# Kernel optimization log

Hardware: AMD Instinct MI355X
Metric: run time of the kernel (lower is better)

## Reference

```python
import jax, jax.numpy as jnp
import numpy as np

NEURON_CDECAY = 0.5
NEURON_VDECAY = 0.75
NEURON_VTH = 0.5
PSEUDO_WINDOW = 0.5

@jax.custom_vjp
def pseudo_spike(v):
    return (v > NEURON_VTH).astype(v.dtype)

def _ps_fwd(v):
    return pseudo_spike(v), v

def _ps_bwd(v, g):
    return (g * (jnp.abs(v - NEURON_VTH) < PSEUDO_WINDOW).astype(g.dtype),)

pseudo_spike.defvjp(_ps_fwd, _ps_bwd)

def clif_scan(X_tbd):
    # X_tbd: [T, B, D] synaptic inputs; CLIF neuron recurrence over time.
    def step(carry, x_t):
        c, v, s = carry
        c = c * NEURON_CDECAY + x_t
        v = v * NEURON_VDECAY * (1.0 - s) + c
        s = pseudo_spike(v)
        return (c, v, s), s
    z = jnp.zeros(X_tbd.shape[1:], X_tbd.dtype)
    _, spikes = jax.lax.scan(step, (z, z, z), X_tbd)
    return spikes  # [T, B, D]

def setup_inputs() -> dict:
    key = jax.random.key(0)
    ks = jax.random.split(key, 8)
    B, IN, H1, H2, OUT, T = 256, 2048, 2048, 2048, 1024, 16
    def lin(k, fan_in, fan_out):
        bound = 1.0 / np.sqrt(fan_in)
        kw, kb = jax.random.split(k)
        W = jax.random.uniform(kw, (fan_out, fan_in), jnp.float32, -bound, bound)
        b = jax.random.uniform(kb, (fan_out,), jnp.float32, -bound, bound)
        return W, b
    W0, b0 = lin(ks[0], IN, H1)
    W1, b1 = lin(ks[1], H1, H2)
    W_out, b_out = lin(ks[2], H2, OUT)
    in_pop_spikes = (jax.random.uniform(ks[3], (B, IN, T), jnp.float32) < 0.5).astype(jnp.float32)
    return {"in_pop_spikes": in_pop_spikes, "W0": W0, "b0": b0, "W1": W1, "b1": b1,
            "W_out": W_out, "b_out": b_out, "batch_size": B, "update": 0, "re_calibration": 0}

def reference(in_pop_spikes, W0, b0, W1, b1, W_out, b_out, batch_size, update, re_calibration):
    # layer 0: linear over all timesteps, then CLIF scan
    x = jnp.moveaxis(in_pop_spikes, -1, 0)                    # [T, B, IN]
    s0 = clif_scan(jnp.einsum('tbi,hi->tbh', x, W0) + b0)     # [T, B, H1]
    s1 = clif_scan(jnp.einsum('tbh,gh->tbg', s0, W1) + b1)    # [T, B, H2]
    so = clif_scan(jnp.einsum('tbg,og->tbo', s1, W_out) + b_out)  # [T, B, OUT]
    return jnp.mean(so, axis=0)  # out_pop_act: sum over T / spike_ts
```

## Files before the change

### kernel.cpp

```cpp
#include <hip/hip_runtime.h>
#include <stdint.h>


typedef int v4i __attribute__((ext_vector_type(4)));
typedef int v16i __attribute__((ext_vector_type(16)));

#define TT 16
constexpr int KD = 2048;
constexpr double SCALE = 268435456.0;
constexpr double BAND = 3.5e-5;
constexpr uint32_t FCAP = 262144;

#define GLOAD_LDS16(g, s)                                                      \
  __builtin_amdgcn_global_load_lds(                                            \
      (const __attribute__((address_space(1))) uint32_t*)(g),                  \
      (__attribute__((address_space(3))) uint32_t*)(s), 16, 0, 0)

__device__ __forceinline__ size_t af_addr(int m, int k) {
  return ((size_t)((m >> 5) * 64 + (k >> 5)) << 10)
       + ((size_t)((m & 31) + (((k >> 4) & 1) << 5)) << 4) + (k & 15);
}

__global__ __launch_bounds__(256)
void prep_all(const float* __restrict__ W0, const float* __restrict__ W1,
              const float* __restrict__ Wo, int8_t* __restrict__ F0,
              int8_t* __restrict__ F1, int8_t* __restrict__ Fo,
              const float* __restrict__ X, int8_t* __restrict__ AF0,
              uint32_t* fl0, uint32_t* fl1, uint32_t* fl2) {
  if (blockIdx.x == 0 && threadIdx.x < 3) {
    if (threadIdx.x == 0) fl0[0] = 0;
    else if (threadIdx.x == 1) fl1[0] = 0;
    else fl2[0] = 0;
  }
  int blk = blockIdx.x;
  if (blk >= 2560) {
    const int idx = (blk - 2560) * 256 + threadIdx.x;
    const float4* src = reinterpret_cast<const float4*>(X) + (size_t)idx * 4;
    float4 v[4];
    v[0] = src[0]; v[1] = src[1]; v[2] = src[2]; v[3] = src[3];
    const float* f = reinterpret_cast<const float*>(v);
    const int b = idx >> 11, i = idx & 2047;
    const size_t base = af_addr(b * TT, i);
#pragma unroll
    for (int t = 0; t < TT; ++t) AF0[base + (size_t)t * 16] = (int8_t)f[t];
    return;
  }
  const float* W;
  int8_t* dst;
  int total;
  if (blk < 1024)      { W = W0; dst = F0; total = 2048 * 2048; }
  else if (blk < 2048) { W = W1; dst = F1; total = 2048 * 2048; blk -= 1024; }
  else                 { W = Wo; dst = Fo; total = 1024 * 2048; blk -= 2048; }
  const int g = blk * 256 + threadIdx.x;
  const int lane = g & 63;
  const int n = ((g >> 12) << 5) + (lane & 31);
  const int k0 = (((g & 4095) >> 6) << 5) + ((lane >> 5) << 4);
  const float* src = W + (size_t)n * 2048 + k0;
  float4 wv[4];
#pragma unroll
  for (int q = 0; q < 4; ++q) wv[q] = *reinterpret_cast<const float4*>(src + q * 4);
  const float* f = reinterpret_cast<const float*>(wv);
  long long nn[16];
#pragma unroll
  for (int e = 0; e < 16; ++e) nn[e] = (long long)rint((double)f[e] * SCALE);
  const size_t base = (size_t)g * 16;
#pragma unroll
  for (int l = 0; l < 3; ++l) {
    alignas(16) char c[16];
#pragma unroll
    for (int e = 0; e < 16; ++e) {
      const int d = (int)((nn[e] + 128) & 255) - 128;
      c[e] = (char)d;
      nn[e] = (nn[e] - d) >> 8;
    }
    *reinterpret_cast<v4i*>(dst + (size_t)l * total + base) = *(const v4i*)c;
  }
}

static __device__ __forceinline__ v16i zero16() {
  v16i z;
#pragma unroll
  for (int i = 0; i < 16; ++i) z[i] = 0;
  return z;
}

template<int N, bool FINAL>
__global__ __launch_bounds__(256, 2)
void gemm_scan_i8(const int8_t* __restrict__ AF,
                  const int8_t* __restrict__ WF,
                  const float* __restrict__ bias,
                  void* __restrict__ outp,
                  uint32_t* __restrict__ fb) {
  __shared__ union SM {
    int8_t buf[3][20 * 1024];
    double c[4][32 * 33];
  } sm;

  const int tid = threadIdx.x;
  const int lane = tid & 63;
  const int w = tid >> 6;
  const int wy = w >> 1, nsub = w & 1;

  if ((blockIdx.x >> 8) & 1) asm volatile("s_sleep 16");

  constexpr int NN = N / 64;
  constexpr int NWG = 32 * NN;
  const int h = blockIdx.x;
  const int wk = (h & 7) * (NWG >> 3) + (h >> 3);
  const int panel = wk >> 6;
  const int within = wk & 63;
  const int mt = (panel & 3) * 8 + (within & 7);
  const int nt = (panel >> 2) * 8 + (within >> 3);
  const int m0 = mt * 128;
  const int n0 = nt * 64;
  const size_t lst = (size_t)N * KD;

  const int8_t* asrc[2];
  int adst[2];
#pragma unroll
  for (int j = 0; j < 2; ++j) {
    const int fa = w + 4 * j;
    asrc[j] = AF + ((size_t)(((m0 >> 5) + (fa >> 1)) * 64 + (fa & 1)) << 10)
            + lane * 16;
    adst[j] = fa * 1024;
  }
  const int8_t* bsrc[3];
  int bdst[3];
#pragma unroll
  for (int j = 0; j < 3; ++j) {
    const int f = w + 4 * j;
    const int l = f >> 2, kk = (f >> 1) & 1, ns = f & 1;
    bsrc[j] = WF + (size_t)l * lst
            + ((size_t)(((n0 >> 5) + ns) * 64 + kk) << 10) + lane * 16;
    bdst[j] = (8 + f) * 1024;
  }

  v16i acc[3][2];
#pragma unroll
  for (int l = 0; l < 3; ++l) { acc[l][0] = zero16(); acc[l][1] = zero16(); }

  constexpr int NT2 = KD / 64;

#pragma unroll
  for (int j = 0; j < 2; ++j) GLOAD_LDS16(asrc[j], &sm.buf[0][adst[j]]);
#pragma unroll
  for (int j = 0; j < 3; ++j) GLOAD_LDS16(bsrc[j], &sm.buf[0][bdst[j]]);
#pragma unroll
  for (int j = 0; j < 2; ++j) GLOAD_LDS16(asrc[j] + 2048, &sm.buf[1][adst[j]]);
#pragma unroll
  for (int j = 0; j < 3; ++j) GLOAD_LDS16(bsrc[j] + 2048, &sm.buf[1][bdst[j]]);

#define GATE()                                                                 \
  __builtin_amdgcn_s_barrier();                                                \
  asm volatile("s_waitcnt lgkmcnt(0)" ::: "memory");                           \
  __builtin_amdgcn_sched_barrier(0)

#define MFMA4(L, BF)                                                           \
  __builtin_amdgcn_s_setprio(1);                                               \
  acc[L][0] = __builtin_amdgcn_mfma_i32_32x32x32_i8(afr[0][0], BF[0], acc[L][0], 0, 0, 0); \
  acc[L][1] = __builtin_amdgcn_mfma_i32_32x32x32_i8(afr[1][0], BF[0], acc[L][1], 0, 0, 0); \
  acc[L][0] = __builtin_amdgcn_mfma_i32_32x32x32_i8(afr[0][1], BF[1], acc[L][0], 0, 0, 0); \
  acc[L][1] = __builtin_amdgcn_mfma_i32_32x32x32_i8(afr[1][1], BF[1], acc[L][1], 0, 0, 0); \
  __builtin_amdgcn_s_setprio(0)

#define BREAD(BF, L)                                                           \
  BF[0] = *(const v4i*)(bb + ((8 + (((L) << 2) | nsub)) << 10) + lane * 16);   \
  BF[1] = *(const v4i*)(bb + ((8 + (((L) << 2) | 2 | nsub)) << 10) + lane * 16)

  int bufc = 0;
  for (int t2 = 0; t2 < NT2; ++t2) {
    if (t2 == NT2 - 1) asm volatile("s_waitcnt vmcnt(0)" ::: "memory");
    else               asm volatile("s_waitcnt vmcnt(5)" ::: "memory");
    __builtin_amdgcn_s_barrier();
    const int8_t* bb = sm.buf[bufc];
    int b2 = bufc + 2; if (b2 >= 3) b2 -= 3;
    const bool stage = (t2 + 2 < NT2);
    const size_t soff = (size_t)(t2 + 2) * 2048;

    v4i afr[2][2], bf0[2], bf1[2];
    if (stage) {
      GLOAD_LDS16(asrc[0] + soff, &sm.buf[b2][adst[0]]);
      GLOAD_LDS16(asrc[1] + soff, &sm.buf[b2][adst[1]]);
    }
#pragma unroll
    for (int mi = 0; mi < 2; ++mi)
#pragma unroll
      for (int kk = 0; kk < 2; ++kk)
        afr[mi][kk] = *(const v4i*)(bb + ((((wy * 2 + mi) << 1) | kk) << 10)
                                       + lane * 16);
    BREAD(bf0, 0);
    GATE();
    MFMA4(0, bf0);

    if (stage) {
      GLOAD_LDS16(bsrc[0] + soff, &sm.buf[b2][bdst[0]]);
      GLOAD_LDS16(bsrc[1] + soff, &sm.buf[b2][bdst[1]]);
    }
    BREAD(bf1, 1);
    GATE();
    MFMA4(1, bf1);

    if (stage) {
      GLOAD_LDS16(bsrc[2] + soff, &sm.buf[b2][bdst[2]]);
    }
    BREAD(bf0, 2);
    GATE();
    MFMA4(2, bf0);

    ++bufc; if (bufc == 3) bufc = 0;
  }
#undef BREAD
#undef MFMA4
#undef GATE

  const int rep = (lane & 31) * 0x01010101;
  v4i rowv; rowv[0] = rep; rowv[1] = rep; rowv[2] = rep; rowv[3] = rep;
  v4i onev; onev[0] = 0x01010101; onev[1] = 0x01010101;
            onev[2] = 0x01010101; onev[3] = 0x01010101;
  const v16i drow = __builtin_amdgcn_mfma_i32_32x32x32_i8(rowv, onev, zero16(), 0, 0, 0);
  const v16i dcol = __builtin_amdgcn_mfma_i32_32x32x32_i8(onev, rowv, zero16(), 0, 0, 0);

  const int col = lane & 31;
  const int bl = lane >> 5;
  double* cw = sm.c[w];
#pragma unroll
  for (int mi = 0; mi < 2; ++mi) {
    __syncthreads();
#pragma unroll
    for (int i = 0; i < 16; ++i) {
      long long ts = acc[2][mi][i];
      ts = (ts << 8) + acc[1][mi][i];
      ts = (ts << 8) + acc[0][mi][i];
      cw[(drow[i] >> 5) * 33 + (dcol[i] >> 5)] = (double)ts * 0x1p-28;
    }
    __syncthreads();

    const int gn = n0 + nsub * 32 + col;
    const int gm = m0 + (wy * 2 + mi) * 32 + bl * 16;
    const double bj = (double)bias[gn];
    double cc = 0.0, vv = 0.0, ss = 0.0;
    int flg = 0;
    if (!FINAL) {
      int8_t* so = (int8_t*)outp;
      const size_t ab = af_addr(gm, gn);
#pragma unroll
      for (int t = 0; t < TT; ++t) {
        const double x = cw[(bl * 16 + t) * 33 + col] + bj;
        cc = cc * 0.5 + x;
        vv = vv * 0.75 * (1.0 - ss) + cc;
        ss = (vv > 0.5) ? 1.0 : 0.0;
        flg |= (fabs(vv - 0.5) < BAND);
        so[ab + (size_t)t * 16] = (int8_t)ss;
      }
    } else {
      float tot = 0.0f;
#pragma unroll
      for (int t = 0; t < TT; ++t) {
        const double x = cw[(bl * 16 + t) * 33 + col] + bj;
        cc = cc * 0.5 + x;
        vv = vv * 0.75 * (1.0 - ss) + cc;
        ss = (vv > 0.5) ? 1.0 : 0.0;
        flg |= (fabs(vv - 0.5) < BAND);
        tot += (float)ss;
      }
      ((float*)outp)[(size_t)(gm / TT) * N + gn] = tot * 0.0625f;
    }
    if (flg) {
      const uint32_t idx = atomicAdd(&fb[0], 1u);
      if (idx < FCAP)
        fb[16 + idx] = ((uint32_t)(gm >> 4) << 11) | (uint32_t)gn;
    }
  }
}

template<int N, bool FINAL>
__global__ __launch_bounds__(256)
void fixup(const int8_t* __restrict__ AFin, const float* __restrict__ W,
           const float* __restrict__ bias, void* __restrict__ outp,
           const uint32_t* __restrict__ fb) {
  const int lane = threadIdx.x & 63;
  const int wv = (blockIdx.x << 2) + (threadIdx.x >> 6);
  const int nw = gridDim.x << 2;
  const uint32_t cnt = fb[0] < FCAP ? fb[0] : FCAP;
  for (uint32_t e = wv; e < cnt; e += nw) {
    const uint32_t ent = fb[16 + e];
    const int b = (int)(ent >> 11), n = (int)(ent & 2047);
    float wq[32];
#pragma unroll
    for (int q = 0; q < 8; ++q)
      *reinterpret_cast<float4*>(&wq[q * 4]) =
          *reinterpret_cast<const float4*>(W + (size_t)n * KD + 32 * lane + 4 * q);
    const int mb = (b & 1) * 16;
    const int8_t* tb = AFin + ((size_t)((b >> 1) * 64 + lane) << 10) + mb * 16;
    double dot[TT];
#pragma unroll
    for (int t = 0; t < TT; ++t) dot[t] = 0.0;
#pragma unroll
    for (int klo = 0; klo < 2; ++klo)
#pragma unroll
      for (int t = 0; t < TT; ++t) {
        v4i sv = *(const v4i*)(tb + (t + 32 * klo) * 16);
        const int8_t* sb = (const int8_t*)&sv;
#pragma unroll
        for (int eidx = 0; eidx < 16; ++eidx)
          dot[t] += sb[eidx] ? (double)wq[klo * 16 + eidx] : 0.0;
      }
#pragma unroll
    for (int t = 0; t < TT; ++t) {
#pragma unroll
      for (int off = 32; off >= 1; off >>= 1)
        dot[t] += __shfl_xor(dot[t], off);
    }
    if (lane == 0) {
      const double bj = (double)bias[n];
      double cc = 0.0, vv = 0.0, ss = 0.0;
      if (!FINAL) {
        int8_t* so = (int8_t*)outp;
#pragma unroll
        for (int t = 0; t < TT; ++t) {
          cc = cc * 0.5 + (dot[t] + bj);
          vv = vv * 0.75 * (1.0 - ss) + cc;
          ss = (vv > 0.5) ? 1.0 : 0.0;
          so[af_addr(TT * b + t, n)] = (int8_t)ss;
        }
      } else {
        float tot = 0.0f;
#pragma unroll
        for (int t = 0; t < TT; ++t) {
          cc = cc * 0.5 + (dot[t] + bj);
          vv = vv * 0.75 * (1.0 - ss) + cc;
          ss = (vv > 0.5) ? 1.0 : 0.0;
          tot += (float)ss;
        }
        ((float*)outp)[(size_t)b * N + n] = tot * 0.0625f;
      }
    }
  }
}

extern "C" void kernel_launch(void* const* d_in, const int* in_sizes, int n_in,
                              void* d_out, int out_size, void* d_ws, size_t ws_size,
                              hipStream_t stream) {
  const float* X  = (const float*)d_in[0];
  const float* W0 = (const float*)d_in[1];
  const float* b0 = (const float*)d_in[2];
  const float* W1 = (const float*)d_in[3];
  const float* b1 = (const float*)d_in[4];
  const float* Wo = (const float*)d_in[5];
  const float* bo = (const float*)d_in[6];
  float* out = (float*)d_out;

  int8_t* base = (int8_t*)d_ws;
  int8_t* AF0 = base;
  int8_t* AF1 = base + (size_t)8388608;
  int8_t* AF2 = AF0;
  int8_t* F0  = base + (size_t)16777216;
  int8_t* F1  = base + (size_t)29360128;
  int8_t* Fo  = base + (size_t)41943040;
  uint32_t* FL0 = (uint32_t*)(base + (size_t)48234496);
  uint32_t* FL1 = (uint32_t*)(base + (size_t)49334272);
  uint32_t* FL2 = (uint32_t*)(base + (size_t)50434048);

  prep_all<<<4608, 256, 0, stream>>>(W0, W1, Wo, F0, F1, Fo, X, AF0,
                                     FL0, FL1, FL2);

  gemm_scan_i8<2048, false><<<1024, 256, 0, stream>>>(AF0, F0, b0, AF1, FL0);
  fixup<2048, false><<<256, 256, 0, stream>>>(AF0, W0, b0, AF1, FL0);
  gemm_scan_i8<2048, false><<<1024, 256, 0, stream>>>(AF1, F1, b1, AF2, FL1);
  fixup<2048, false><<<256, 256, 0, stream>>>(AF1, W1, b1, AF2, FL1);
  gemm_scan_i8<1024, true ><<< 512, 256, 0, stream>>>(AF2, Fo, bo, out, FL2);
  fixup<1024, true ><<<256, 256, 0, stream>>>(AF2, Wo, bo, out, FL2);
}
```

Measured before the change: 193.9 us.

## Load A fragments directly to registers and give each wave private B buffers

Reworks the GEMM main loop so each wave streams its own B fragments into a private triple-buffered LDS region, while A fragments are loaded straight from global memory into registers with double buffering. This removes the block-wide barriers between MFMA groups and the shared A staging in LDS. It also drops the staggered s_sleep start. B is now loaded redundantly per wave (duplicated across wy pairs), so global/L2 traffic rises, and A is read from global memory by each wave pair without LDS sharing.

New measurement: 238.0 us. 1.23x slower.

```diff
diff --git a/kernel.cpp b/kernel.cpp
--- a/kernel.cpp
+++ b/kernel.cpp
@@ -92,7 +92,7 @@
                   void* __restrict__ outp,
                   uint32_t* __restrict__ fb) {
   __shared__ union SM {
-    int8_t buf[3][20 * 1024];
+    int8_t buf[4][18 * 1024];
     double c[4][32 * 33];
   } sm;
 
@@ -100,8 +100,6 @@
   const int lane = tid & 63;
   const int w = tid >> 6;
   const int wy = w >> 1, nsub = w & 1;
-
-  if ((blockIdx.x >> 8) & 1) asm volatile("s_sleep 16");
 
   constexpr int NN = N / 64;
   constexpr int NWG = 32 * NN;
@@ -115,25 +113,19 @@
   const int n0 = nt * 64;
   const size_t lst = (size_t)N * KD;
 
-  const int8_t* asrc[2];
-  int adst[2];
-#pragma unroll
-  for (int j = 0; j < 2; ++j) {
-    const int fa = w + 4 * j;
-    asrc[j] = AF + ((size_t)(((m0 >> 5) + (fa >> 1)) * 64 + (fa & 1)) << 10)
-            + lane * 16;
-    adst[j] = fa * 1024;
-  }
-  const int8_t* bsrc[3];
-  int bdst[3];
-#pragma unroll
-  for (int j = 0; j < 3; ++j) {
-    const int f = w + 4 * j;
-    const int l = f >> 2, kk = (f >> 1) & 1, ns = f & 1;
-    bsrc[j] = WF + (size_t)l * lst
-            + ((size_t)(((n0 >> 5) + ns) * 64 + kk) << 10) + lane * 16;
-    bdst[j] = (8 + f) * 1024;
-  }
+  const int8_t* bsrc[6];
+#pragma unroll
+  for (int l = 0; l < 3; ++l)
+#pragma unroll
+    for (int kk = 0; kk < 2; ++kk)
+      bsrc[l * 2 + kk] = WF + (size_t)l * lst
+          + ((size_t)(((n0 >> 5) + nsub) * 64 + kk) << 10) + lane * 16;
+  int8_t* wbuf = sm.buf[w];
+
+  const int8_t* aP[2];
+#pragma unroll
+  for (int mi = 0; mi < 2; ++mi)
+    aP[mi] = AF + ((size_t)((m0 >> 5) + wy * 2 + mi) << 16) + lane * 16;
 
   v16i acc[3][2];
 #pragma unroll
@@ -142,76 +134,66 @@
   constexpr int NT2 = KD / 64;
 
 #pragma unroll
-  for (int j = 0; j < 2; ++j) GLOAD_LDS16(asrc[j], &sm.buf[0][adst[j]]);
-#pragma unroll
-  for (int j = 0; j < 3; ++j) GLOAD_LDS16(bsrc[j], &sm.buf[0][bdst[j]]);
-#pragma unroll
-  for (int j = 0; j < 2; ++j) GLOAD_LDS16(asrc[j] + 2048, &sm.buf[1][adst[j]]);
-#pragma unroll
-  for (int j = 0; j < 3; ++j) GLOAD_LDS16(bsrc[j] + 2048, &sm.buf[1][bdst[j]]);
-
-#define GATE()                                                                 \
-  __builtin_amdgcn_s_barrier();                                                \
-  asm volatile("s_waitcnt lgkmcnt(0)" ::: "memory");                           \
-  __builtin_amdgcn_sched_barrier(0)
-
-#define MFMA4(L, BF)                                                           \
-  __builtin_amdgcn_s_setprio(1);                                               \
-  acc[L][0] = __builtin_amdgcn_mfma_i32_32x32x32_i8(afr[0][0], BF[0], acc[L][0], 0, 0, 0); \
-  acc[L][1] = __builtin_amdgcn_mfma_i32_32x32x32_i8(afr[1][0], BF[0], acc[L][1], 0, 0, 0); \
-  acc[L][0] = __builtin_amdgcn_mfma_i32_32x32x32_i8(afr[0][1], BF[1], acc[L][0], 0, 0, 0); \
-  acc[L][1] = __builtin_amdgcn_mfma_i32_32x32x32_i8(afr[1][1], BF[1], acc[L][1], 0, 0, 0); \
-  __builtin_amdgcn_s_setprio(0)
-
-#define BREAD(BF, L)                                                           \
-  BF[0] = *(const v4i*)(bb + ((8 + (((L) << 2) | nsub)) << 10) + lane * 16);   \
-  BF[1] = *(const v4i*)(bb + ((8 + (((L) << 2) | 2 | nsub)) << 10) + lane * 16)
+  for (int fr = 0; fr < 6; ++fr) GLOAD_LDS16(bsrc[fr], wbuf + fr * 1024);
+  v4i aA[2][2], aB[2][2];
+#pragma unroll
+  for (int mi = 0; mi < 2; ++mi)
+#pragma unroll
+    for (int kk = 0; kk < 2; ++kk)
+      aA[mi][kk] = *(const v4i*)(aP[mi] + kk * 1024);
+#pragma unroll
+  for (int fr = 0; fr < 6; ++fr)
+    GLOAD_LDS16(bsrc[fr] + 2048, wbuf + 6144 + fr * 1024);
 
   int bufc = 0;
-  for (int t2 = 0; t2 < NT2; ++t2) {
-    if (t2 == NT2 - 1) asm volatile("s_waitcnt vmcnt(0)" ::: "memory");
-    else               asm volatile("s_waitcnt vmcnt(5)" ::: "memory");
-    __builtin_amdgcn_s_barrier();
-    const int8_t* bb = sm.buf[bufc];
-    int b2 = bufc + 2; if (b2 >= 3) b2 -= 3;
-    const bool stage = (t2 + 2 < NT2);
-    const size_t soff = (size_t)(t2 + 2) * 2048;
-
-    v4i afr[2][2], bf0[2], bf1[2];
-    if (stage) {
-      GLOAD_LDS16(asrc[0] + soff, &sm.buf[b2][adst[0]]);
-      GLOAD_LDS16(asrc[1] + soff, &sm.buf[b2][adst[1]]);
-    }
-#pragma unroll
-    for (int mi = 0; mi < 2; ++mi)
-#pragma unroll
-      for (int kk = 0; kk < 2; ++kk)
-        afr[mi][kk] = *(const v4i*)(bb + ((((wy * 2 + mi) << 1) | kk) << 10)
-                                       + lane * 16);
-    BREAD(bf0, 0);
-    GATE();
-    MFMA4(0, bf0);
-
-    if (stage) {
-      GLOAD_LDS16(bsrc[0] + soff, &sm.buf[b2][bdst[0]]);
-      GLOAD_LDS16(bsrc[1] + soff, &sm.buf[b2][bdst[1]]);
-    }
-    BREAD(bf1, 1);
-    GATE();
-    MFMA4(1, bf1);
-
-    if (stage) {
-      GLOAD_LDS16(bsrc[2] + soff, &sm.buf[b2][bdst[2]]);
-    }
-    BREAD(bf0, 2);
-    GATE();
-    MFMA4(2, bf0);
-
-    ++bufc; if (bufc == 3) bufc = 0;
-  }
-#undef BREAD
-#undef MFMA4
-#undef GATE
+
+#define BODY(T, AUSE, ALOAD)                                                   \
+  {                                                                            \
+    const int t_ = (T);                                                        \
+    if (t_ == NT2 - 1) asm volatile("s_waitcnt vmcnt(0)" ::: "memory");        \
+    else               asm volatile("s_waitcnt vmcnt(6)" ::: "memory");        \
+    const int8_t* bb_ = wbuf + bufc * 6144;                                    \
+    v4i bf_[3][2];                                                             \
+    _Pragma("unroll")                                                          \
+    for (int l = 0; l < 3; ++l)                                                \
+      _Pragma("unroll")                                                        \
+      for (int kk = 0; kk < 2; ++kk)                                           \
+        bf_[l][kk] = *(const v4i*)(bb_ + ((l * 2 + kk) << 10) + lane * 16);    \
+    asm volatile("s_waitcnt lgkmcnt(0)" ::: "memory");                         \
+    __builtin_amdgcn_sched_barrier(0);                                         \
+    if (t_ + 1 < NT2) {                                                        \
+      _Pragma("unroll")                                                        \
+      for (int mi = 0; mi < 2; ++mi)                                           \
+        _Pragma("unroll")                                                      \
+        for (int kk = 0; kk < 2; ++kk)                                         \
+          ALOAD[mi][kk] = *(const v4i*)(aP[mi] + ((t_ + 1) * 2 + kk) * 1024);  \
+    }                                                                          \
+    if (t_ + 2 < NT2) {                                                        \
+      int b2_ = bufc + 2; if (b2_ >= 3) b2_ -= 3;                              \
+      _Pragma("unroll")                                                        \
+      for (int fr = 0; fr < 6; ++fr)                                           \
+        GLOAD_LDS16(bsrc[fr] + (size_t)(t_ + 2) * 2048,                        \
+                    wbuf + b2_ * 6144 + fr * 1024);                            \
+    }                                                                          \
+    __builtin_amdgcn_s_setprio(1);                                             \
+    _Pragma("unroll")                                                          \
+    for (int l = 0; l < 3; ++l)                                                \
+      _Pragma("unroll")                                                        \
+      for (int kk = 0; kk < 2; ++kk) {                                         \
+        acc[l][0] = __builtin_amdgcn_mfma_i32_32x32x32_i8(AUSE[0][kk],         \
+                        bf_[l][kk], acc[l][0], 0, 0, 0);                       \
+        acc[l][1] = __builtin_amdgcn_mfma_i32_32x32x32_i8(AUSE[1][kk],         \
+                        bf_[l][kk], acc[l][1], 0, 0, 0);                       \
+      }                                                                        \
+    __builtin_amdgcn_s_setprio(0);                                             \
+    ++bufc; if (bufc == 3) bufc = 0;                                           \
+  }
+
+  for (int t2 = 0; t2 < NT2; t2 += 2) {
+    BODY(t2,     aA, aB);
+    BODY(t2 + 1, aB, aA);
+  }
+#undef BODY
 
   const int rep = (lane & 31) * 0x01010101;
   v4i rowv; rowv[0] = rep; rowv[1] = rep; rowv[2] = rep; rowv[3] = rep;
```

## Enlarge GEMM tile to 128x128 with single-phase MFMA loop per K step

Applied to the files above, without the earlier changes.

Doubles the N tile from 64 to 128, so each wave computes a 2x2 block of 32x32 outputs per limb instead of 2x1. A fragments are reused across twice as many columns, and the grid is halved. The three interleaved load/barrier/MFMA phases per K step become one bulk staging call followed by all LDS reads and 24 MFMAs. LDS per buffer grows to 32KB with launch bounds of 1 block per CU, trading occupancy and in-loop overlap for fewer barriers and better reuse. The s_sleep stagger for odd block groups is removed.

Measured after the change: 211.8 us. +9.2%, slower.

```diff
diff --git a/kernel.cpp b/kernel.cpp
--- a/kernel.cpp
+++ b/kernel.cpp
@@ -85,26 +85,24 @@
 }
 
 template<int N, bool FINAL>
-__global__ __launch_bounds__(256, 2)
+__global__ __launch_bounds__(256, 1)
 void gemm_scan_i8(const int8_t* __restrict__ AF,
                   const int8_t* __restrict__ WF,
                   const float* __restrict__ bias,
                   void* __restrict__ outp,
                   uint32_t* __restrict__ fb) {
   __shared__ union SM {
-    int8_t buf[3][20 * 1024];
+    int8_t buf[3][32 * 1024];
     double c[4][32 * 33];
   } sm;
 
   const int tid = threadIdx.x;
   const int lane = tid & 63;
   const int w = tid >> 6;
-  const int wy = w >> 1, nsub = w & 1;
-
-  if ((blockIdx.x >> 8) & 1) asm volatile("s_sleep 16");
-
-  constexpr int NN = N / 64;
-  constexpr int NWG = 32 * NN;
+  const int wy = w >> 1, wx = w & 1;
+
+  constexpr int NT = N / 128;
+  constexpr int NWG = 32 * NT;
   const int h = blockIdx.x;
   const int wk = (h & 7) * (NWG >> 3) + (h >> 3);
   const int panel = wk >> 6;
@@ -112,7 +110,7 @@
   const int mt = (panel & 3) * 8 + (within & 7);
   const int nt = (panel >> 2) * 8 + (within >> 3);
   const int m0 = mt * 128;
-  const int n0 = nt * 64;
+  const int n0 = nt * 128;
   const size_t lst = (size_t)N * KD;
 
   const int8_t* asrc[2];
@@ -124,94 +122,84 @@
             + lane * 16;
     adst[j] = fa * 1024;
   }
-  const int8_t* bsrc[3];
-  int bdst[3];
-#pragma unroll
-  for (int j = 0; j < 3; ++j) {
+  const int8_t* bsrc[6];
+  int bdst[6];
+#pragma unroll
+  for (int j = 0; j < 6; ++j) {
     const int f = w + 4 * j;
-    const int l = f >> 2, kk = (f >> 1) & 1, ns = f & 1;
+    const int l = f >> 3, ntl = (f >> 1) & 3, kk = f & 1;
     bsrc[j] = WF + (size_t)l * lst
-            + ((size_t)(((n0 >> 5) + ns) * 64 + kk) << 10) + lane * 16;
+            + ((size_t)(((n0 >> 5) + ntl) * 64 + kk) << 10) + lane * 16;
     bdst[j] = (8 + f) * 1024;
   }
 
-  v16i acc[3][2];
-#pragma unroll
-  for (int l = 0; l < 3; ++l) { acc[l][0] = zero16(); acc[l][1] = zero16(); }
+#define STAGE(T, BUF)                                                          \
+  {                                                                            \
+    _Pragma("unroll")                                                          \
+    for (int j = 0; j < 2; ++j)                                                \
+      GLOAD_LDS16(asrc[j] + (size_t)(T) * 2048, &sm.buf[BUF][adst[j]]);        \
+    _Pragma("unroll")                                                          \
+    for (int j = 0; j < 6; ++j)                                                \
+      GLOAD_LDS16(bsrc[j] + (size_t)(T) * 2048, &sm.buf[BUF][bdst[j]]);        \
+  }
+
+  v16i acc[3][2][2];
+#pragma unroll
+  for (int l = 0; l < 3; ++l)
+#pragma unroll
+    for (int mi = 0; mi < 2; ++mi)
+#pragma unroll
+      for (int ni = 0; ni < 2; ++ni) acc[l][mi][ni] = zero16();
 
   constexpr int NT2 = KD / 64;
 
-#pragma unroll
-  for (int j = 0; j < 2; ++j) GLOAD_LDS16(asrc[j], &sm.buf[0][adst[j]]);
-#pragma unroll
-  for (int j = 0; j < 3; ++j) GLOAD_LDS16(bsrc[j], &sm.buf[0][bdst[j]]);
-#pragma unroll
-  for (int j = 0; j < 2; ++j) GLOAD_LDS16(asrc[j] + 2048, &sm.buf[1][adst[j]]);
-#pragma unroll
-  for (int j = 0; j < 3; ++j) GLOAD_LDS16(bsrc[j] + 2048, &sm.buf[1][bdst[j]]);
-
-#define GATE()                                                                 \
-  __builtin_amdgcn_s_barrier();                                                \
-  asm volatile("s_waitcnt lgkmcnt(0)" ::: "memory");                           \
-  __builtin_amdgcn_sched_barrier(0)
-
-#define MFMA4(L, BF)                                                           \
-  __builtin_amdgcn_s_setprio(1);                                               \
-  acc[L][0] = __builtin_amdgcn_mfma_i32_32x32x32_i8(afr[0][0], BF[0], acc[L][0], 0, 0, 0); \
-  acc[L][1] = __builtin_amdgcn_mfma_i32_32x32x32_i8(afr[1][0], BF[0], acc[L][1], 0, 0, 0); \
-  acc[L][0] = __builtin_amdgcn_mfma_i32_32x32x32_i8(afr[0][1], BF[1], acc[L][0], 0, 0, 0); \
-  acc[L][1] = __builtin_amdgcn_mfma_i32_32x32x32_i8(afr[1][1], BF[1], acc[L][1], 0, 0, 0); \
-  __builtin_amdgcn_s_setprio(0)
-
-#define BREAD(BF, L)                                                           \
-  BF[0] = *(const v4i*)(bb + ((8 + (((L) << 2) | nsub)) << 10) + lane * 16);   \
-  BF[1] = *(const v4i*)(bb + ((8 + (((L) << 2) | 2 | nsub)) << 10) + lane * 16)
+  STAGE(0, 0);
+  STAGE(1, 1);
 
   int bufc = 0;
   for (int t2 = 0; t2 < NT2; ++t2) {
     if (t2 == NT2 - 1) asm volatile("s_waitcnt vmcnt(0)" ::: "memory");
-    else               asm volatile("s_waitcnt vmcnt(5)" ::: "memory");
+    else               asm volatile("s_waitcnt vmcnt(8)" ::: "memory");
     __builtin_amdgcn_s_barrier();
+    if (t2 + 2 < NT2) {
+      int b2 = bufc + 2; if (b2 >= 3) b2 -= 3;
+      STAGE(t2 + 2, b2);
+    }
     const int8_t* bb = sm.buf[bufc];
-    int b2 = bufc + 2; if (b2 >= 3) b2 -= 3;
-    const bool stage = (t2 + 2 < NT2);
-    const size_t soff = (size_t)(t2 + 2) * 2048;
-
-    v4i afr[2][2], bf0[2], bf1[2];
-    if (stage) {
-      GLOAD_LDS16(asrc[0] + soff, &sm.buf[b2][adst[0]]);
-      GLOAD_LDS16(asrc[1] + soff, &sm.buf[b2][adst[1]]);
-    }
+
+    v4i afr[2][2], bfr[3][2][2];
 #pragma unroll
     for (int mi = 0; mi < 2; ++mi)
 #pragma unroll
       for (int kk = 0; kk < 2; ++kk)
         afr[mi][kk] = *(const v4i*)(bb + ((((wy * 2 + mi) << 1) | kk) << 10)
                                        + lane * 16);
-    BREAD(bf0, 0);
-    GATE();
-    MFMA4(0, bf0);
-
-    if (stage) {
-      GLOAD_LDS16(bsrc[0] + soff, &sm.buf[b2][bdst[0]]);
-      GLOAD_LDS16(bsrc[1] + soff, &sm.buf[b2][bdst[1]]);
-    }
-    BREAD(bf1, 1);
-    GATE();
-    MFMA4(1, bf1);
-
-    if (stage) {
-      GLOAD_LDS16(bsrc[2] + soff, &sm.buf[b2][bdst[2]]);
-    }
-    BREAD(bf0, 2);
-    GATE();
-    MFMA4(2, bf0);
-
+#pragma unroll
+    for (int l = 0; l < 3; ++l)
+#pragma unroll
+      for (int ni = 0; ni < 2; ++ni)
+#pragma unroll
+        for (int kk = 0; kk < 2; ++kk)
+          bfr[l][ni][kk] = *(const v4i*)(bb
+              + ((8 + ((l << 3) | ((wx * 2 + ni) << 1) | kk)) << 10)
+              + lane * 16);
+    asm volatile("s_waitcnt lgkmcnt(0)" ::: "memory");
+    __builtin_amdgcn_sched_barrier(0);
+    __builtin_amdgcn_s_setprio(1);
+#pragma unroll
+    for (int kk = 0; kk < 2; ++kk)
+#pragma unroll
+      for (int l = 0; l < 3; ++l)
+#pragma unroll
+        for (int mi = 0; mi < 2; ++mi)
+#pragma unroll
+          for (int ni = 0; ni < 2; ++ni)
+            acc[l][mi][ni] = __builtin_amdgcn_mfma_i32_32x32x32_i8(
+                afr[mi][kk], bfr[l][ni][kk], acc[l][mi][ni], 0, 0, 0);
+    __builtin_amdgcn_s_setprio(0);
     ++bufc; if (bufc == 3) bufc = 0;
   }
-#undef BREAD
-#undef MFMA4
-#undef GATE
+#undef STAGE
 
   const int rep = (lane & 31) * 0x01010101;
   v4i rowv; rowv[0] = rep; rowv[1] = rep; rowv[2] = rep; rowv[3] = rep;
@@ -224,53 +212,55 @@
   const int bl = lane >> 5;
   double* cw = sm.c[w];
 #pragma unroll
-  for (int mi = 0; mi < 2; ++mi) {
-    __syncthreads();
-#pragma unroll
-    for (int i = 0; i < 16; ++i) {
-      long long ts = acc[2][mi][i];
-      ts = (ts << 8) + acc[1][mi][i];
-      ts = (ts << 8) + acc[0][mi][i];
-      cw[(drow[i] >> 5) * 33 + (dcol[i] >> 5)] = (double)ts * 0x1p-28;
-    }
-    __syncthreads();
-
-    const int gn = n0 + nsub * 32 + col;
-    const int gm = m0 + (wy * 2 + mi) * 32 + bl * 16;
-    const double bj = (double)bias[gn];
-    double cc = 0.0, vv = 0.0, ss = 0.0;
-    int flg = 0;
-    if (!FINAL) {
-      int8_t* so = (int8_t*)outp;
-      const size_t ab = af_addr(gm, gn);
-#pragma unroll
-      for (int t = 0; t < TT; ++t) {
-        const double x = cw[(bl * 16 + t) * 33 + col] + bj;
-        cc = cc * 0.5 + x;
-        vv = vv * 0.75 * (1.0 - ss) + cc;
-        ss = (vv > 0.5) ? 1.0 : 0.0;
-        flg |= (fabs(vv - 0.5) < BAND);
-        so[ab + (size_t)t * 16] = (int8_t)ss;
-      }
-    } else {
-      float tot = 0.0f;
-#pragma unroll
-      for (int t = 0; t < TT; ++t) {
-        const double x = cw[(bl * 16 + t) * 33 + col] + bj;
-        cc = cc * 0.5 + x;
-        vv = vv * 0.75 * (1.0 - ss) + cc;
-        ss = (vv > 0.5) ? 1.0 : 0.0;
-        flg |= (fabs(vv - 0.5) < BAND);
-        tot += (float)ss;
-      }
-      ((float*)outp)[(size_t)(gm / TT) * N + gn] = tot * 0.0625f;
-    }
-    if (flg) {
-      const uint32_t idx = atomicAdd(&fb[0], 1u);
-      if (idx < FCAP)
-        fb[16 + idx] = ((uint32_t)(gm >> 4) << 11) | (uint32_t)gn;
-    }
-  }
+  for (int mi = 0; mi < 2; ++mi)
+#pragma unroll
+    for (int ni = 0; ni < 2; ++ni) {
+      __syncthreads();
+#pragma unroll
+      for (int i = 0; i < 16; ++i) {
+        long long ts = acc[2][mi][ni][i];
+        ts = (ts << 8) + acc[1][mi][ni][i];
+        ts = (ts << 8) + acc[0][mi][ni][i];
+        cw[(drow[i] >> 5) * 33 + (dcol[i] >> 5)] = (double)ts * 0x1p-28;
+      }
+      __syncthreads();
+
+      const int gn = n0 + (wx * 2 + ni) * 32 + col;
+      const int gm = m0 + (wy * 2 + mi) * 32 + bl * 16;
+      const double bj = (double)bias[gn];
+      double cc = 0.0, vv = 0.0, ss = 0.0;
+      int flg = 0;
+      if (!FINAL) {
+        int8_t* so = (int8_t*)outp;
+        const size_t ab = af_addr(gm, gn);
+#pragma unroll
+        for (int t = 0; t < TT; ++t) {
+          const double x = cw[(bl * 16 + t) * 33 + col] + bj;
+          cc = cc * 0.5 + x;
+          vv = vv * 0.75 * (1.0 - ss) + cc;
+          ss = (vv > 0.5) ? 1.0 : 0.0;
+          flg |= (fabs(vv - 0.5) < BAND);
+          so[ab + (size_t)t * 16] = (int8_t)ss;
+        }
+      } else {
+        float tot = 0.0f;
+#pragma unroll
+        for (int t = 0; t < TT; ++t) {
+          const double x = cw[(bl * 16 + t) * 33 + col] + bj;
+          cc = cc * 0.5 + x;
+          vv = vv * 0.75 * (1.0 - ss) + cc;
+          ss = (vv > 0.5) ? 1.0 : 0.0;
+          flg |= (fabs(vv - 0.5) < BAND);
+          tot += (float)ss;
+        }
+        ((float*)outp)[(size_t)(gm / TT) * N + gn] = tot * 0.0625f;
+      }
+      if (flg) {
+        const uint32_t idx = atomicAdd(&fb[0], 1u);
+        if (idx < FCAP)
+          fb[16 + idx] = ((uint32_t)(gm >> 4) << 11) | (uint32_t)gn;
+      }
+    }
 }
 
 template<int N, bool FINAL>
@@ -364,10 +354,10 @@
   prep_all<<<4608, 256, 0, stream>>>(W0, W1, Wo, F0, F1, Fo, X, AF0,
                                      FL0, FL1, FL2);
 
-  gemm_scan_i8<2048, false><<<1024, 256, 0, stream>>>(AF0, F0, b0, AF1, FL0);
+  gemm_scan_i8<2048, false><<<512, 256, 0, stream>>>(AF0, F0, b0, AF1, FL0);
   fixup<2048, false><<<256, 256, 0, stream>>>(AF0, W0, b0, AF1, FL0);
-  gemm_scan_i8<2048, false><<<1024, 256, 0, stream>>>(AF1, F1, b1, AF2, FL1);
+  gemm_scan_i8<2048, false><<<512, 256, 0, stream>>>(AF1, F1, b1, AF2, FL1);
   fixup<2048, false><<<256, 256, 0, stream>>>(AF1, W1, b1, AF2, FL1);
-  gemm_scan_i8<1024, true ><<< 512, 256, 0, stream>>>(AF2, Fo, bo, out, FL2);
+  gemm_scan_i8<1024, true ><<<256, 256, 0, stream>>>(AF2, Fo, bo, out, FL2);
   fixup<1024, true ><<<256, 256, 0, stream>>>(AF2, Wo, bo, out, FL2);
 }
```
